# Kernel optimization log

Measured on AMD Instinct MI355X. Metric: run time of the kernel, lower is better.

The kernel has to match this reference:

```python
import jax, jax.numpy as jnp
import numpy as np

DEGREE = 3


def bspline_basis(t, knots, degree):
    """Vectorized Cox-de Boor recursion. t: [S], knots: [K]. Returns B: [S, K-degree-1].
    Faithful to the torch loop: at degree d only columns [0, n_knots-d) are updated;
    higher columns keep their stale lower-degree values, and term2 reads the
    not-yet-updated column i+1 (i.e. previous-degree values), matching ascending-i
    in-place updates.
    """
    n_knots = knots.shape[0] - degree - 1
    # degree-0 basis: indicator of half-open knot spans
    B = ((knots[None, :n_knots] <= t[:, None]) &
         (t[:, None] < knots[None, 1:n_knots + 1])).astype(t.dtype)
    for d in range(1, degree + 1):
        n = n_knots - d
        denom1 = knots[d:d + n] - knots[:n]          # knots[i+d]   - knots[i]
        denom2 = knots[d + 1:d + 1 + n] - knots[1:1 + n]  # knots[i+d+1] - knots[i+1]
        safe1 = jnp.where(denom1 == 0, 1.0, denom1)
        safe2 = jnp.where(denom2 == 0, 1.0, denom2)
        w1 = jnp.where(denom1 == 0, 0.0, (t[:, None] - knots[None, :n]) / safe1)
        w2 = jnp.where(denom2 == 0, 0.0, (knots[None, d + 1:d + 1 + n] - t[:, None]) / safe2)
        new_cols = w1 * B[:, :n] + w2 * B[:, 1:n + 1]
        B = B.at[:, :n].set(new_cols)
    return B


def setup_inputs() -> dict:
    key = jax.random.key(0)
    k1, k2 = jax.random.split(key)
    N_KNOTS, DIM, T_MAX = 2048, 512, 32768.0
    t = jnp.sort(jax.random.uniform(k1, (N_KNOTS,), dtype=jnp.float32)) * T_MAX
    t = t.at[-1].set(T_MAX)  # make sample range exactly [0, T_MAX)
    c = jax.random.normal(k2, (DIM, N_KNOTS), dtype=jnp.float32)
    return {"t": t, "c": c, "delta": 1}


def reference(t, c, delta):
    padded_t = jnp.concatenate([jnp.zeros(DEGREE + 1, dtype=t.dtype), t])
    # number of samples is data-dependent (t[-1]); concretize outside jit
    t_max = float(t[-1])
    sample_points = jnp.arange(0.0, t_max, float(delta), dtype=t.dtype)  # [S]
    B = bspline_basis(sample_points, padded_t, DEGREE)  # [S, n_knots]
    spline_values = B @ c.T  # [S, dim]
    return sample_points, spline_values
```

## Files before the change

kernel.cpp:

```cpp
#include <hip/hip_runtime.h>


#define DEG 3

typedef float vfloat4 __attribute__((ext_vector_type(4)));

__device__ __forceinline__ float kn(const float* __restrict__ t, int i) {
    return (i < DEG + 1) ? 0.0f : t[i - (DEG + 1)];
}

#define TILE 32
__global__ __launch_bounds__(256) void prep_kernel(
    const float* __restrict__ c, float* __restrict__ cT,
    const float* __restrict__ t, const int* __restrict__ delta_p,
    float* __restrict__ out_pts, int* __restrict__ jbuf,
    vfloat4* __restrict__ bbuf, int S, int NK, int DIM, int TB)
{
    if ((int)blockIdx.x < TB) {
        __shared__ float tile[TILE][TILE + 1];
        int bx = blockIdx.x % (NK / TILE);
        int by = blockIdx.x / (NK / TILE);
        int tx = threadIdx.x % TILE;
        int ty = threadIdx.x / TILE;
        int x = bx * TILE + tx;
        int y = by * TILE + ty;
        #pragma unroll
        for (int i = 0; i < TILE; i += 8)
            tile[ty + i][tx] = c[(size_t)(y + i) * NK + x];
        __syncthreads();
        int x2 = by * TILE + tx;
        int y2 = bx * TILE + ty;
        #pragma unroll
        for (int i = 0; i < TILE; i += 8)
            cT[(size_t)(y2 + i) * DIM + x2] = tile[tx][ty + i];
        return;
    }

    int s = (blockIdx.x - TB) * blockDim.x + threadIdx.x;
    if (s >= S) return;
    const float delta = (float)(*delta_p);
    const float sv = (float)s * delta;
    out_pts[s] = sv;

    int lo = DEG, hi = NK + DEG - 1;
    while (lo < hi) {
        int mid = (lo + hi + 1) >> 1;
        if (kn(t, mid) <= sv) lo = mid; else hi = mid - 1;
    }
    const int j = lo;

    if (j >= NK) {
        jbuf[s] = NK - 1;
        bbuf[s] = (vfloat4){0.f, 0.f, 0.f, 0.f};
        return;
    }

    float N[DEG + 1][DEG + 1];
    N[0][0] = 1.0f;
    #pragma unroll
    for (int d = 1; d <= DEG; ++d) {
        #pragma unroll
        for (int k = 0; k <= d; ++k) {
            int i = j - d + k;
            float vpi  = (k >= 1) ? N[d - 1][k - 1] : 0.0f;
            float vpi1 = (k <= d - 1) ? N[d - 1][k] : 0.0f;
            float ki   = kn(t, i);
            float kid  = kn(t, i + d);
            float ki1  = kn(t, i + 1);
            float kid1 = kn(t, i + d + 1);
            float den1 = kid - ki;
            float den2 = kid1 - ki1;
            float w1 = (den1 != 0.0f) ? (sv - ki) / den1 : 0.0f;
            float w2 = (den2 != 0.0f) ? (kid1 - sv) / den2 : 0.0f;
            N[d][k] = w1 * vpi + w2 * vpi1;
        }
    }

    float b[DEG + 1];
    #pragma unroll
    for (int m = 0; m <= DEG; ++m) {
        int col = j - DEG + m;
        int deg = NK - 1 - col; if (deg > DEG) deg = DEG;
        int idx = m - DEG + deg;
        b[m] = (idx >= 0) ? N[deg][idx] : 0.0f;
    }
    jbuf[s] = j;
    bbuf[s] = (vfloat4){b[0], b[1], b[2], b[3]};
}

__device__ __forceinline__ vfloat4 dot4(const vfloat4 b, const vfloat4 a0,
                                        const vfloat4 a1, const vfloat4 a2,
                                        const vfloat4 a3) {
    return b.x * a0 + b.y * a1 + b.z * a2 + b.w * a3;
}

__global__ __launch_bounds__(256) void bspline_eval(
    const int* __restrict__ jbuf, const vfloat4* __restrict__ bbuf,
    const float* __restrict__ cT, vfloat4* __restrict__ out_spline,
    int DIM)
{
    const int nvec = DIM >> 2;
    int gtid = blockIdx.x * blockDim.x + threadIdx.x;
    int wid  = gtid >> 6;
    int lane = gtid & 63;
    int grp  = wid >> 1;
    int d    = ((wid & 1) << 6) | lane;
    int s0   = __builtin_amdgcn_readfirstlane(grp << 2);

    const int j0 = jbuf[s0 + 0];
    const int j3 = jbuf[s0 + 3];
    const vfloat4 b0 = bbuf[s0 + 0];
    const vfloat4 b1 = bbuf[s0 + 1];
    const vfloat4 b2 = bbuf[s0 + 2];
    const vfloat4 b3 = bbuf[s0 + 3];

    vfloat4* o = out_spline + (size_t)s0 * nvec + d;

    if (j0 == j3) {
        const vfloat4* r = (const vfloat4*)(cT + (size_t)(j3 - 3) * DIM) + d;
        vfloat4 a0 = r[0];
        vfloat4 a1 = r[nvec];
        vfloat4 a2 = r[2 * nvec];
        vfloat4 a3 = r[3 * nvec];
        __builtin_nontemporal_store(dot4(b0, a0, a1, a2, a3), o);
        __builtin_nontemporal_store(dot4(b1, a0, a1, a2, a3), o + nvec);
        __builtin_nontemporal_store(dot4(b2, a0, a1, a2, a3), o + 2 * nvec);
        __builtin_nontemporal_store(dot4(b3, a0, a1, a2, a3), o + 3 * nvec);
    } else {
        const int j1 = jbuf[s0 + 1];
        const int j2 = jbuf[s0 + 2];
        const int js[4] = {j0, j1, j2, j3};
        const vfloat4 bs[4] = {b0, b1, b2, b3};
        #pragma unroll
        for (int m = 0; m < 4; ++m) {
            const vfloat4* r = (const vfloat4*)(cT + (size_t)(js[m] - 3) * DIM) + d;
            vfloat4 a0 = r[0];
            vfloat4 a1 = r[nvec];
            vfloat4 a2 = r[2 * nvec];
            vfloat4 a3 = r[3 * nvec];
            __builtin_nontemporal_store(dot4(bs[m], a0, a1, a2, a3), o + m * nvec);
        }
    }
}

extern "C" void kernel_launch(void* const* d_in, const int* in_sizes, int n_in,
                              void* d_out, int out_size, void* d_ws, size_t ws_size,
                              hipStream_t stream) {
    const float* t = (const float*)d_in[0];
    const float* c = (const float*)d_in[1];
    const int* delta = (const int*)d_in[2];
    const int NK = in_sizes[0];
    const int DIM = in_sizes[1] / NK;
    const int S = out_size / (1 + DIM);

    float* cT = (float*)d_ws;
    int* jbuf = (int*)((char*)d_ws + (size_t)NK * DIM * 4);
    vfloat4* bbuf = (vfloat4*)((char*)jbuf + (size_t)S * 4);

    const int TB = (NK / TILE) * (DIM / TILE);
    const int WB = (S + 255) / 256;
    prep_kernel<<<TB + WB, 256, 0, stream>>>(
        c, cT, t, delta, (float*)d_out, jbuf, bbuf, S, NK, DIM, TB);

    int total_threads = (S >> 2) * (DIM >> 2);
    bspline_eval<<<total_threads / 256, 256, 0, stream>>>(
        jbuf, bbuf, cT, (vfloat4*)((float*)d_out + S), DIM);
}
```

Measured before the change: 95.47 us.

## Fuse basis computation, coefficient gather and evaluation into one tiled kernel

Replaces the two-kernel pipeline (global transpose of c plus basis precompute, then evaluation) with a single kernel. Each block computes knot spans and basis weights for 128 samples, stages the needed coefficient columns for a 128-wide dim chunk into shared memory, then evaluates from LDS. This drops the transpose pass, the intermediate jbuf/bbuf round trip and one launch. The cost is that the binary search and basis computation are repeated once per dim chunk, and there is a slow global-memory fallback when a sample block spans more than 64 knot columns.

```diff
diff --git a/kernel.cpp b/kernel.cpp
--- a/kernel.cpp
+++ b/kernel.cpp
@@ -2,6 +2,10 @@
 
 
 #define DEG 3
+#define SBLK 128
+#define DBLK 128
+#define NCOLS 64
+#define CSTRIDE (DBLK + 4)
 
 typedef float vfloat4 __attribute__((ext_vector_type(4)));
 
@@ -9,137 +13,116 @@
     return (i < DEG + 1) ? 0.0f : t[i - (DEG + 1)];
 }
 
-#define TILE 32
-__global__ __launch_bounds__(256) void prep_kernel(
-    const float* __restrict__ c, float* __restrict__ cT,
-    const float* __restrict__ t, const int* __restrict__ delta_p,
-    float* __restrict__ out_pts, int* __restrict__ jbuf,
-    vfloat4* __restrict__ bbuf, int S, int NK, int DIM, int TB)
+__global__ __launch_bounds__(256) void bspline_fused(
+    const float* __restrict__ t, const float* __restrict__ c,
+    const int* __restrict__ delta_p, float* __restrict__ out_pts,
+    vfloat4* __restrict__ out_spline, int S, int NK, int DIM, int nd)
 {
-    if ((int)blockIdx.x < TB) {
-        __shared__ float tile[TILE][TILE + 1];
-        int bx = blockIdx.x % (NK / TILE);
-        int by = blockIdx.x / (NK / TILE);
-        int tx = threadIdx.x % TILE;
-        int ty = threadIdx.x / TILE;
-        int x = bx * TILE + tx;
-        int y = by * TILE + ty;
-        #pragma unroll
-        for (int i = 0; i < TILE; i += 8)
-            tile[ty + i][tx] = c[(size_t)(y + i) * NK + x];
-        __syncthreads();
-        int x2 = by * TILE + tx;
-        int y2 = bx * TILE + ty;
-        #pragma unroll
-        for (int i = 0; i < TILE; i += 8)
-            cT[(size_t)(y2 + i) * DIM + x2] = tile[tx][ty + i];
-        return;
+    __shared__ __attribute__((aligned(16))) float lc[NCOLS][CSTRIDE];
+    __shared__ vfloat4 bwS[SBLK];
+    __shared__ int jS[SBLK];
+
+    const int tid = threadIdx.x;
+    const int dchunk = blockIdx.x % nd;
+    const int sb = blockIdx.x / nd;
+    const int s0 = sb * SBLK;
+    const int dbase = dchunk * DBLK;
+
+    if (tid < SBLK) {
+        const int s = s0 + tid;
+        const int sc = (s < S) ? s : (S - 1);
+        const float delta = (float)(*delta_p);
+        const float sv = (float)sc * delta;
+        if (dchunk == 0 && s < S) out_pts[s] = sv;
+
+        int lo = DEG, hi = NK + DEG - 1;
+        while (lo < hi) {
+            int mid = (lo + hi + 1) >> 1;
+            if (kn(t, mid) <= sv) lo = mid; else hi = mid - 1;
+        }
+        int j = lo;
+        vfloat4 b4 = (vfloat4){0.f, 0.f, 0.f, 0.f};
+        if (j < NK) {
+            float N[DEG + 1][DEG + 1];
+            N[0][0] = 1.0f;
+            #pragma unroll
+            for (int d = 1; d <= DEG; ++d) {
+                #pragma unroll
+                for (int k = 0; k <= d; ++k) {
+                    int i = j - d + k;
+                    float vpi  = (k >= 1) ? N[d - 1][k - 1] : 0.0f;
+                    float vpi1 = (k <= d - 1) ? N[d - 1][k] : 0.0f;
+                    float ki   = kn(t, i);
+                    float kid  = kn(t, i + d);
+                    float ki1  = kn(t, i + 1);
+                    float kid1 = kn(t, i + d + 1);
+                    float den1 = kid - ki;
+                    float den2 = kid1 - ki1;
+                    float w1 = (den1 != 0.0f) ? (sv - ki) / den1 : 0.0f;
+                    float w2 = (den2 != 0.0f) ? (kid1 - sv) / den2 : 0.0f;
+                    N[d][k] = w1 * vpi + w2 * vpi1;
+                }
+            }
+            float b[DEG + 1];
+            #pragma unroll
+            for (int m = 0; m <= DEG; ++m) {
+                int col = j - DEG + m;
+                int deg = NK - 1 - col; if (deg > DEG) deg = DEG;
+                int idx = m - DEG + deg;
+                b[m] = (idx >= 0) ? N[deg][idx] : 0.0f;
+            }
+            b4 = (vfloat4){b[0], b[1], b[2], b[3]};
+        } else {
+            j = NK - 1;
+        }
+        jS[tid] = j;
+        bwS[tid] = b4;
     }
+    __syncthreads();
 
-    int s = (blockIdx.x - TB) * blockDim.x + threadIdx.x;
-    if (s >= S) return;
-    const float delta = (float)(*delta_p);
-    const float sv = (float)s * delta;
-    out_pts[s] = sv;
+    const int colmin = jS[0] - DEG;
+    int nc = jS[SBLK - 1] - colmin + 1;
+    if (nc > NCOLS) nc = NCOLS;
+    int ncr = 16, lsh = 4;
+    while (ncr < nc) { ncr <<= 1; ++lsh; }
+    for (int e = tid; e < ncr * DBLK; e += 256) {
+        int cc = e & (ncr - 1);
+        int dd = e >> lsh;
+        int col = colmin + cc;
+        if (col > NK - 1) col = NK - 1;
+        lc[cc][dd] = c[(size_t)(dbase + dd) * NK + col];
+    }
+    __syncthreads();
 
-    int lo = DEG, hi = NK + DEG - 1;
-    while (lo < hi) {
-        int mid = (lo + hi + 1) >> 1;
-        if (kn(t, mid) <= sv) lo = mid; else hi = mid - 1;
-    }
-    const int j = lo;
-
-    if (j >= NK) {
-        jbuf[s] = NK - 1;
-        bbuf[s] = (vfloat4){0.f, 0.f, 0.f, 0.f};
-        return;
-    }
-
-    float N[DEG + 1][DEG + 1];
-    N[0][0] = 1.0f;
+    const int nv = DIM >> 2;
+    vfloat4* ob = out_spline + (size_t)s0 * nv + (dbase >> 2);
     #pragma unroll
-    for (int d = 1; d <= DEG; ++d) {
-        #pragma unroll
-        for (int k = 0; k <= d; ++k) {
-            int i = j - d + k;
-            float vpi  = (k >= 1) ? N[d - 1][k - 1] : 0.0f;
-            float vpi1 = (k <= d - 1) ? N[d - 1][k] : 0.0f;
-            float ki   = kn(t, i);
-            float kid  = kn(t, i + d);
-            float ki1  = kn(t, i + 1);
-            float kid1 = kn(t, i + d + 1);
-            float den1 = kid - ki;
-            float den2 = kid1 - ki1;
-            float w1 = (den1 != 0.0f) ? (sv - ki) / den1 : 0.0f;
-            float w2 = (den2 != 0.0f) ? (kid1 - sv) / den2 : 0.0f;
-            N[d][k] = w1 * vpi + w2 * vpi1;
+    for (int k = 0; k < (SBLK * (DBLK >> 2)) / 256; ++k) {
+        const int it = k * 256 + tid;
+        const int sl = it >> 5;
+        const int d4 = it & 31;
+        const int j = jS[sl];
+        const vfloat4 b = bwS[sl];
+        const int cl = j - DEG - colmin;
+        vfloat4 r;
+        if (cl + DEG < NCOLS) {
+            const float* p = &lc[cl][d4 << 2];
+            vfloat4 a0 = *(const vfloat4*)(p);
+            vfloat4 a1 = *(const vfloat4*)(p + CSTRIDE);
+            vfloat4 a2 = *(const vfloat4*)(p + 2 * CSTRIDE);
+            vfloat4 a3 = *(const vfloat4*)(p + 3 * CSTRIDE);
+            r = b.x * a0 + b.y * a1 + b.z * a2 + b.w * a3;
+        } else {
+            float rv[4];
+            #pragma unroll
+            for (int q = 0; q < 4; ++q) {
+                const float* cq = c + (size_t)(dbase + (d4 << 2) + q) * NK + (j - DEG);
+                rv[q] = b.x * cq[0] + b.y * cq[1] + b.z * cq[2] + b.w * cq[3];
+            }
+            r = (vfloat4){rv[0], rv[1], rv[2], rv[3]};
         }
-    }
-
-    float b[DEG + 1];
-    #pragma unroll
-    for (int m = 0; m <= DEG; ++m) {
-        int col = j - DEG + m;
-        int deg = NK - 1 - col; if (deg > DEG) deg = DEG;
-        int idx = m - DEG + deg;
-        b[m] = (idx >= 0) ? N[deg][idx] : 0.0f;
-    }
-    jbuf[s] = j;
-    bbuf[s] = (vfloat4){b[0], b[1], b[2], b[3]};
-}
-
-__device__ __forceinline__ vfloat4 dot4(const vfloat4 b, const vfloat4 a0,
-                                        const vfloat4 a1, const vfloat4 a2,
-                                        const vfloat4 a3) {
-    return b.x * a0 + b.y * a1 + b.z * a2 + b.w * a3;
-}
-
-__global__ __launch_bounds__(256) void bspline_eval(
-    const int* __restrict__ jbuf, const vfloat4* __restrict__ bbuf,
-    const float* __restrict__ cT, vfloat4* __restrict__ out_spline,
-    int DIM)
-{
-    const int nvec = DIM >> 2;
-    int gtid = blockIdx.x * blockDim.x + threadIdx.x;
-    int wid  = gtid >> 6;
-    int lane = gtid & 63;
-    int grp  = wid >> 1;
-    int d    = ((wid & 1) << 6) | lane;
-    int s0   = __builtin_amdgcn_readfirstlane(grp << 2);
-
-    const int j0 = jbuf[s0 + 0];
-    const int j3 = jbuf[s0 + 3];
-    const vfloat4 b0 = bbuf[s0 + 0];
-    const vfloat4 b1 = bbuf[s0 + 1];
-    const vfloat4 b2 = bbuf[s0 + 2];
-    const vfloat4 b3 = bbuf[s0 + 3];
-
-    vfloat4* o = out_spline + (size_t)s0 * nvec + d;
-
-    if (j0 == j3) {
-        const vfloat4* r = (const vfloat4*)(cT + (size_t)(j3 - 3) * DIM) + d;
-        vfloat4 a0 = r[0];
-        vfloat4 a1 = r[nvec];
-        vfloat4 a2 = r[2 * nvec];
-        vfloat4 a3 = r[3 * nvec];
-        __builtin_nontemporal_store(dot4(b0, a0, a1, a2, a3), o);
-        __builtin_nontemporal_store(dot4(b1, a0, a1, a2, a3), o + nvec);
-        __builtin_nontemporal_store(dot4(b2, a0, a1, a2, a3), o + 2 * nvec);
-        __builtin_nontemporal_store(dot4(b3, a0, a1, a2, a3), o + 3 * nvec);
-    } else {
-        const int j1 = jbuf[s0 + 1];
-        const int j2 = jbuf[s0 + 2];
-        const int js[4] = {j0, j1, j2, j3};
-        const vfloat4 bs[4] = {b0, b1, b2, b3};
-        #pragma unroll
-        for (int m = 0; m < 4; ++m) {
-            const vfloat4* r = (const vfloat4*)(cT + (size_t)(js[m] - 3) * DIM) + d;
-            vfloat4 a0 = r[0];
-            vfloat4 a1 = r[nvec];
-            vfloat4 a2 = r[2 * nvec];
-            vfloat4 a3 = r[3 * nvec];
-            __builtin_nontemporal_store(dot4(bs[m], a0, a1, a2, a3), o + m * nvec);
-        }
+        if (s0 + sl < S)
+            __builtin_nontemporal_store(r, ob + (size_t)sl * nv + d4);
     }
 }
 
@@ -153,16 +136,9 @@
     const int DIM = in_sizes[1] / NK;
     const int S = out_size / (1 + DIM);
 
-    float* cT = (float*)d_ws;
-    int* jbuf = (int*)((char*)d_ws + (size_t)NK * DIM * 4);
-    vfloat4* bbuf = (vfloat4*)((char*)jbuf + (size_t)S * 4);
-
-    const int TB = (NK / TILE) * (DIM / TILE);
-    const int WB = (S + 255) / 256;
-    prep_kernel<<<TB + WB, 256, 0, stream>>>(
-        c, cT, t, delta, (float*)d_out, jbuf, bbuf, S, NK, DIM, TB);
-
-    int total_threads = (S >> 2) * (DIM >> 2);
-    bspline_eval<<<total_threads / 256, 256, 0, stream>>>(
-        jbuf, bbuf, cT, (vfloat4*)((float*)d_out + S), DIM);
+    const int nd = DIM / DBLK;
+    const int nsb = (S + SBLK - 1) / SBLK;
+    bspline_fused<<<nsb * nd, 256, 0, stream>>>(
+        t, c, delta, (float*)d_out,
+        (vfloat4*)((float*)d_out + S), S, NK, DIM, nd);
 }
```

After: 90.62 us. 1.05x faster.
